# Kernel tuning notes

Measured on AMD Instinct MI355X. Metric: run time of the kernel, lower is better.

## Reference

```python
import jax, jax.numpy as jnp
import numpy as np
import math

DIM = 384
HEADS = 6
HID = 32  # PositionalEncodingFourier hidden_dim
B, H, W = 16, 56, 56


def _layer_norm(x, g, b, eps=1e-6):
    mu = jnp.mean(x, axis=-1, keepdims=True)
    var = jnp.mean((x - mu) ** 2, axis=-1, keepdims=True)
    return (x - mu) * jax.lax.rsqrt(var + eps) * g + b


def _pos_encoding_fourier(Bb, Hh, Ww, w, b):
    # EdgeNeXt PositionalEncodingFourier with all-False mask: cumsum == arange+1
    scale = 2.0 * math.pi
    y_embed = jnp.arange(1, Hh + 1, dtype=jnp.float32)[:, None] / (Hh + 1e-6) * scale
    x_embed = jnp.arange(1, Ww + 1, dtype=jnp.float32)[None, :] / (Ww + 1e-6) * scale
    dim_t = 10000.0 ** (2.0 * (jnp.arange(HID) // 2).astype(jnp.float32) / HID)
    def enc(e):
        p = jnp.broadcast_to(e, (Hh, Ww))[..., None] / dim_t  # (H,W,HID)
        return jnp.stack([jnp.sin(p[..., 0::2]), jnp.cos(p[..., 1::2])], axis=-1).reshape(Hh, Ww, HID)
    pos = jnp.concatenate([enc(y_embed), enc(x_embed)], axis=-1)  # (H,W,2*HID)
    pos = pos @ w.T + b  # 1x1 conv token_projection as matmul -> (H,W,DIM)
    return jnp.broadcast_to(jnp.transpose(pos, (2, 0, 1))[None], (Bb, DIM, Hh, Ww))


def _forward(x, pos_w, pos_b, ln_g, ln_b, gamma_xca, temperature,
             qkv_w, qkv_b, proj_w, proj_b, rpb_table, conv_w,
             bn_g, bn_b, bn_mean, bn_var, gamma):
    Bb, C, Hh, Ww = x.shape
    N = Hh * Ww
    d = C // HEADS
    xt = jnp.transpose(x.reshape(Bb, C, N), (0, 2, 1))  # (B,N,C)
    pos = _pos_encoding_fourier(Bb, Hh, Ww, pos_w, pos_b)
    xt = xt + jnp.transpose(pos.reshape(Bb, C, N), (0, 2, 1))

    # relative position bias (seq_len T=2): gather (T,T,h) -> expand (h,d^2,T,T)
    # -> nearest interp x0.5 selects element (0,0) -> pixel_shuffle(d) of constant
    # channels == per-head scalar broadcast over the (d,d) channel-attention map.
    T = 2
    rel_idx = jnp.arange(T)[:, None] - jnp.arange(T)[None, :] + T - 1  # (2,2)
    rpb = rpb_table[rel_idx.reshape(-1)].reshape(T, T, HEADS)
    bias = rpb[0, 0][None, :, None, None]  # (1,heads,1,1), broadcasts over (d,d)

    # XCA: cross-covariance (channel) attention
    xn = _layer_norm(xt, ln_g, ln_b)
    qkv = (xn @ qkv_w.T + qkv_b).reshape(Bb, N, 3, HEADS, d)
    qkv = jnp.transpose(qkv, (2, 0, 3, 4, 1))  # (3,B,h,d,N)
    q, k, v = qkv[0], qkv[1], qkv[2]
    q = q / jnp.maximum(jnp.linalg.norm(q, axis=-1, keepdims=True), 1e-12)
    k = k / jnp.maximum(jnp.linalg.norm(k, axis=-1, keepdims=True), 1e-12)
    attn = jnp.einsum('bhdn,bhen->bhde', q, k) * temperature + bias  # (B,h,d,d)
    attn = jax.nn.softmax(attn, axis=-1)
    out = jnp.einsum('bhde,bhen->bhdn', attn, v)  # (B,h,d,N)
    out = jnp.transpose(out, (0, 3, 1, 2)).reshape(Bb, N, C)
    out = out @ proj_w.T + proj_b
    xt = xt + gamma_xca * out

    x2 = jnp.transpose(xt, (0, 2, 1)).reshape(Bb, C, Hh, Ww)
    # pwconv0: conv3x3 (dim->dim, expan_ration hardcoded to 1) + BN(inference) + SiLU
    xi = jax.lax.conv_general_dilated(x2, conv_w, (1, 1), [(1, 1), (1, 1)],
                                      dimension_numbers=('NCHW', 'OIHW', 'NCHW'))
    xi = (xi - bn_mean[None, :, None, None]) * jax.lax.rsqrt(bn_var + 1e-5)[None, :, None, None]
    xi = xi * bn_g[None, :, None, None] + bn_b[None, :, None, None]
    xi = xi * jax.nn.sigmoid(xi)  # SiLU
    x2 = x2 + xi

    # faithful to source: raw reshape (NOT permute) of contiguous NCHW into (B,H,W,C)
    x3 = x2.reshape(Bb, Hh, Ww, C) * gamma
    x3 = jnp.transpose(x3, (0, 3, 1, 2))
    return x + x3


def setup_inputs() -> dict:
    key = jax.random.key(0)
    ks = jax.random.split(key, 10)
    d3 = 3 * DIM
    return {
        'x': jax.random.normal(ks[0], (B, DIM, H, W), jnp.float32),
        'pos_w': jax.random.normal(ks[1], (DIM, 2 * HID), jnp.float32) * 0.05,
        'pos_b': jnp.zeros((DIM,), jnp.float32),
        'ln_g': jnp.ones((DIM,), jnp.float32),
        'ln_b': jnp.zeros((DIM,), jnp.float32),
        'gamma_xca': jax.random.normal(ks[2], (DIM,), jnp.float32) * 0.1,
        'temperature': jnp.ones((HEADS, 1, 1), jnp.float32),
        'qkv_w': jax.random.normal(ks[3], (d3, DIM), jnp.float32) * (DIM ** -0.5),
        'qkv_b': jnp.zeros((d3,), jnp.float32),
        'proj_w': jax.random.normal(ks[4], (DIM, DIM), jnp.float32) * (DIM ** -0.5),
        'proj_b': jnp.zeros((DIM,), jnp.float32),
        'rpb_table': jax.random.normal(ks[5], (3, HEADS), jnp.float32) * 0.02,
        'conv_w': jax.random.normal(ks[6], (DIM, DIM, 3, 3), jnp.float32) * 0.02,
        'bn_g': jnp.ones((DIM,), jnp.float32),
        'bn_b': jnp.zeros((DIM,), jnp.float32),
        'bn_mean': jax.random.normal(ks[7], (DIM,), jnp.float32) * 0.1,
        'bn_var': jax.random.uniform(ks[8], (DIM,), jnp.float32, 0.5, 1.5),
        'gamma': jax.random.normal(ks[9], (DIM,), jnp.float32) * 0.1,
    }


def reference(x, pos_w, pos_b, ln_g, ln_b, gamma_xca, temperature,
              qkv_w, qkv_b, proj_w, proj_b, rpb_table, conv_w,
              bn_g, bn_b, bn_mean, bn_var, gamma):
    return _forward(x, pos_w, pos_b, ln_g, ln_b, gamma_xca, temperature,
                    qkv_w, qkv_b, proj_w, proj_b, rpb_table, conv_w,
                    bn_g, bn_b, bn_mean, bn_var, gamma)
```

## Files before the change

### kernel.cpp

```cpp
#include <hip/hip_runtime.h>
#include <hip/hip_bf16.h>
#include <math.h>

#define DIM 384
#define HEADS 6
#define NN 3136
#define BB 16
#define BH (BB*HEADS)
#define HP 58
#define NP (HP*HP)

typedef __attribute__((ext_vector_type(8))) short short8;
typedef __attribute__((ext_vector_type(4))) short short4v;
typedef __attribute__((ext_vector_type(4))) float f32x4;

__device__ __forceinline__ float bf2f(unsigned short u) {
    union { unsigned int i; float f; } v; v.i = ((unsigned int)u) << 16; return v.f;
}
__device__ __forceinline__ unsigned short f2bf(float f) {
    union { float f; unsigned int i; } v; v.f = f;
    unsigned int r = v.i + 0x7fffu + ((v.i >> 16) & 1u);
    return (unsigned short)(r >> 16);
}
__device__ __forceinline__ void glds16(const unsigned short* g, void* l) {
    __builtin_amdgcn_global_load_lds(
        (const __attribute__((address_space(1))) unsigned int*)g,
        (__attribute__((address_space(3))) unsigned int*)l, 16, 0, 0);
}

__global__ void kw_convert(const float* __restrict__ qkv_w, const float* __restrict__ proj_w,
                           const float* __restrict__ conv_w,
                           unsigned short* __restrict__ Wq, unsigned short* __restrict__ Wp,
                           unsigned short* __restrict__ Wc) {
    int tid = blockIdx.x * 256 + threadIdx.x;
    int stride = gridDim.x * 256;
    for (int i = tid; i < 3*DIM*DIM; i += stride) Wq[i] = f2bf(qkv_w[i]);
    for (int i = tid; i < DIM*DIM; i += stride) Wp[i] = f2bf(proj_w[i]);
    for (int i = tid; i < DIM*DIM*9; i += stride) {
        int ii = i % DIM; int rest = i / DIM; int tap = rest % 9; int o = rest / 9;
        Wc[i] = f2bf(conv_w[(size_t)(o*DIM + ii)*9 + tap]);
    }
}

__global__ void k_pos(const float* __restrict__ pos_w, const float* __restrict__ pos_b,
                      float* __restrict__ P) {
    int n = blockIdx.x; int h = n / 56, w = n % 56;
    __shared__ float feat[64];
    int t = threadIdx.x;
    if (t < 64) {
        int axis = t >> 5;
        int k = t & 31; int i = k >> 1;
        float e = (float)((axis ? w : h) + 1) / 56.000001f * 6.28318530717958647692f;
        float arg = e / powf(10000.0f, (float)i / 16.0f);
        feat[t] = (k & 1) ? cosf(arg) : sinf(arg);
    }
    __syncthreads();
    for (int c = t; c < DIM; c += blockDim.x) {
        float s = pos_b[c];
        #pragma unroll 8
        for (int k = 0; k < 64; k++) s += feat[k] * pos_w[c*64 + k];
        P[(size_t)n*DIM + c] = s;
    }
}

__global__ __launch_bounds__(256) void k_tln(const float* __restrict__ x, const float* __restrict__ P,
                                             const float* __restrict__ g, const float* __restrict__ be,
                                             unsigned short* __restrict__ XTb, unsigned short* __restrict__ XN) {
    __shared__ float tile[32][388];
    int blk = blockIdx.x;
    int b = blk / 98, nt = blk % 98;
    int n0 = nt*32;
    int t = threadIdx.x;
    #pragma unroll
    for (int it = 0; it < 12; it++) {
        int task = it*256 + t;
        int c = task >> 3, seg = task & 7;
        float4 v = *reinterpret_cast<const float4*>(x + ((size_t)(b*DIM + c))*NN + n0 + seg*4);
        tile[seg*4+0][c] = v.x; tile[seg*4+1][c] = v.y;
        tile[seg*4+2][c] = v.z; tile[seg*4+3][c] = v.w;
    }
    __syncthreads();
    int row = t >> 3, sub = t & 7;
    int n = n0 + row;
    f32x4 xp[12];
    float s = 0.f;
    #pragma unroll
    for (int k = 0; k < 12; k++) {
        int c0 = (k*8 + sub)*4;
        float4 tv = *reinterpret_cast<float4*>(&tile[row][c0]);
        float4 pv = *reinterpret_cast<const float4*>(P + (size_t)n*DIM + c0);
        f32x4 xv = {tv.x+pv.x, tv.y+pv.y, tv.z+pv.z, tv.w+pv.w};
        xp[k] = xv;
        s += xv[0]+xv[1]+xv[2]+xv[3];
        unsigned short pkx[4];
        #pragma unroll
        for (int e=0;e<4;e++) pkx[e] = f2bf(xv[e]);
        *reinterpret_cast<short4v*>(XTb + ((size_t)(b*NN + n))*DIM + c0) = *(short4v*)pkx;
    }
    s += __shfl_xor(s, 1, 64); s += __shfl_xor(s, 2, 64); s += __shfl_xor(s, 4, 64);
    float mean = s * (1.0f/384.0f);
    float sq = 0.f;
    #pragma unroll
    for (int k = 0; k < 12; k++) {
        #pragma unroll
        for (int e = 0; e < 4; e++) { float d = xp[k][e]-mean; sq += d*d; }
    }
    sq += __shfl_xor(sq, 1, 64); sq += __shfl_xor(sq, 2, 64); sq += __shfl_xor(sq, 4, 64);
    float rs = rsqrtf(sq * (1.0f/384.0f) + 1e-6f);
    #pragma unroll
    for (int k = 0; k < 12; k++) {
        int c0 = (k*8 + sub)*4;
        unsigned short pk[4];
        #pragma unroll
        for (int e = 0; e < 4; e++)
            pk[e] = f2bf((xp[k][e]-mean)*rs*g[c0+e] + be[c0+e]);
        *reinterpret_cast<short4v*>(XN + ((size_t)(b*NN + n))*DIM + c0) = *(short4v*)pk;
    }
}

template<int MODE>
__global__ __launch_bounds__(256) void k_gemm(
    const unsigned short* __restrict__ A, const unsigned short* __restrict__ Wt,
    const float* __restrict__ bias,
    unsigned short* __restrict__ Qb, unsigned short* __restrict__ Kb, unsigned short* __restrict__ Vt,
    const unsigned short* __restrict__ XTb, const float* __restrict__ gxca, unsigned short* __restrict__ X2p)
{
    __shared__ __align__(16) char smem[35328];
    auto ctA = (float(*)[69])smem;
    auto ctB = (float(*)[130])smem;

    constexpr int NCT = (MODE == 0) ? 9 : 3;
    constexpr int CPX = (MODE == 0) ? 441 : 147;
    int bid = blockIdx.x;
    int orig = (bid & 7)*CPX + (bid >> 3);
    int ct = orig % NCT, mt = orig / NCT;
    int m0 = mt*128, o0 = ct*128;
    int t = threadIdx.x;
    int wave = t >> 6, lane = t & 63;
    int wr = wave >> 1, wc = wave & 1;
    int lr = lane & 15, lg = lane >> 4;

    int r0 = t >> 2;
    int swcol = (((t & 3) ^ ((t >> 3) & 3)) << 3);
    const unsigned short* a0 = A  + (size_t)(m0 + r0)*384 + swcol;
    const unsigned short* a1 = A  + (size_t)(m0 + 64 + r0)*384 + swcol;
    const unsigned short* b0 = Wt + (size_t)(o0 + r0)*384 + swcol;
    const unsigned short* b1 = Wt + (size_t)(o0 + 64 + r0)*384 + swcol;
    int rsw = ((lr >> 1) & 3) << 3;

    auto stage = [&](char* base, int c) {
        glds16(a0 + c, base + wave*1024);
        glds16(a1 + c, base + 4096 + wave*1024);
        glds16(b0 + c, base + 8192 + wave*1024);
        glds16(b1 + c, base + 12288 + wave*1024);
    };

    f32x4 acc[4][4];
    #pragma unroll
    for (int i=0;i<4;i++) for (int j=0;j<4;j++) acc[i][j] = (f32x4){0.f,0.f,0.f,0.f};

    stage(smem, 0);
    __syncthreads();
    for (int kk = 0; kk < 12; kk++) {
        if (kk < 11) stage(smem + ((kk+1)&1)*16384, (kk+1)*32);
        auto As = (unsigned short(*)[32])(smem + (kk&1)*16384);
        auto Bs = (unsigned short(*)[32])(smem + (kk&1)*16384 + 8192);
        short8 af[4], bfv[4];
        #pragma unroll
        for (int i=0;i<4;i++) af[i]  = *(short8*)&As[wr*64 + i*16 + lr][(lg*8) ^ rsw];
        #pragma unroll
        for (int j=0;j<4;j++) bfv[j] = *(short8*)&Bs[wc*64 + j*16 + lr][(lg*8) ^ rsw];
        #pragma unroll
        for (int i=0;i<4;i++)
            #pragma unroll
            for (int j=0;j<4;j++)
                acc[i][j] = __builtin_amdgcn_mfma_f32_16x16x32_bf16(af[i], bfv[j], acc[i][j], 0, 0, 0);
        __syncthreads();
    }

    int comp = (MODE == 0) ? (o0 / DIM) : 0;
    for (int mh = 0; mh < 2; mh++) {
        __syncthreads();
        bool useB = (MODE == 1) || (MODE == 0 && comp == 2);
        if (wr == mh) {
            if (useB) {
                #pragma unroll
                for (int i=0;i<4;i++) for (int j=0;j<4;j++) for (int r=0;r<4;r++)
                    ctB[i*16 + lg*4 + r][wc*64 + j*16 + lr] = acc[i][j][r];
            } else {
                #pragma unroll
                for (int i=0;i<4;i++) for (int j=0;j<4;j++) for (int r=0;r<4;r++)
                    ctA[wc*64 + j*16 + lr][i*16 + lg*4 + r] = acc[i][j][r];
            }
        }
        __syncthreads();
        if (MODE == 1) {
            for (int q = t; q < 1024; q += 256) {
                int row = q >> 4, seg = q & 15;
                int m = m0 + mh*64 + row; int b = m/NN; int n = m - b*NN;
                int py = n/56, px = n - py*56;
                int og0 = o0 + seg*8;
                short8 xvb = *(const short8*)(XTb + (size_t)m*DIM + og0);
                unsigned short pk[8];
                #pragma unroll
                for (int e=0;e<8;e++) {
                    float val = ctB[row][seg*8+e] + bias[og0+e];
                    pk[e] = f2bf(bf2f((unsigned short)xvb[e]) + gxca[og0+e]*val);
                }
                *(short8*)(X2p + ((size_t)(b*NP + (py+1)*HP + px + 1))*DIM + og0) = *(short8*)pk;
            }
        } else if (comp < 2) {
            unsigned short* Dst = (comp == 0) ? Qb : Kb;
            for (int q = t; q < 2048; q += 256) {
                int row = q >> 4, seg = q & 15;
                int og = o0 + row; int rem = og - comp*DIM;
                int hh = rem >> 6, dd = rem & 63;
                int m4 = m0 + mh*64 + seg*4; int b = m4/NN; int n = m4 - b*NN;
                float bv = bias[og];
                unsigned short pk[4];
                #pragma unroll
                for (int e=0;e<4;e++) pk[e] = f2bf(ctA[row][seg*4+e] + bv);
                *(short4v*)(Dst + ((size_t)((b*HEADS + hh)*64 + dd))*NN + n) = *(short4v*)pk;
            }
        } else {
            for (int q = t; q < 1024; q += 256) {
                int row = q >> 4, seg = q & 15;
                int m = m0 + mh*64 + row; int b = m/NN; int n = m - b*NN;
                int og0 = o0 + seg*8; int rem0 = og0 - 2*DIM;
                int hh = rem0 >> 6, dd0 = rem0 & 63;
                unsigned short pk[8];
                #pragma unroll
                for (int e=0;e<8;e++) pk[e] = f2bf(ctB[row][seg*8+e] + bias[og0+e]);
                *(short8*)(Vt + ((size_t)((b*HEADS + hh)*NN + n))*64 + dd0) = *(short8*)pk;
            }
        }
    }
}

__global__ __launch_bounds__(256) void k_pad(unsigned short* __restrict__ X2p) {
    int b = blockIdx.x, part = blockIdx.y;
    unsigned short* base = X2p + (size_t)b*NP*DIM;
    short8 z = {0,0,0,0,0,0,0,0};
    for (int task = part*256 + threadIdx.x; task < 10944; task += 2048) {
        int pos = task / 48, seg = task - pos*48;
        int py, px;
        if (pos < 58)       { py = 0;  px = pos; }
        else if (pos < 116) { py = 57; px = pos - 58; }
        else if (pos < 172) { py = pos - 115; px = 0; }
        else                { py = pos - 171; px = 57; }
        *(short8*)(base + ((size_t)(py*HP + px))*DIM + seg*8) = z;
    }
}

__global__ __launch_bounds__(512) void k_conv(
    const unsigned short* __restrict__ A, const unsigned short* __restrict__ Wt,
    const float* __restrict__ bn_g, const float* __restrict__ bn_b,
    const float* __restrict__ bn_mean, const float* __restrict__ bn_var,
    float* __restrict__ Yout)
{
    __shared__ __align__(16) char smem[32768];
    auto ctA = (float(*)[69])smem;
    auto X2s = (unsigned short(*)[68])(smem + 17664);

    int bid = blockIdx.x;
    int orig = (bid & 7)*150 + (bid >> 3);
    int ct = orig % 3; int rest = orig / 3;
    int tile = rest % 25; int b = rest / 25;
    int n0 = tile*128, o0 = ct*128;
    int t = threadIdx.x;
    int wave = t >> 6, lane = t & 63;
    int wr = wave >> 2, wc = wave & 3;
    int lr = lane & 15, lg = lane >> 4;
    int qb = n0 + 2*(n0/56);
    const size_t bbase = (size_t)b*NP*DIM;

    int swcol = (((t & 3) ^ ((t >> 3) & 3)) << 3);
    const unsigned short* asrc[2];
    #pragma unroll
    for (int j=0;j<2;j++) {
        int row = j*128 + (t >> 2);
        int q = qb + row; if (q > NP-1) q = NP-1;
        asrc[j] = A + bbase + (size_t)q*DIM + swcol;
    }
    const unsigned short* bsrc = Wt + (size_t)(o0 + (t >> 2))*3456 + swcol;

    int qrel[4];
    #pragma unroll
    for (int i=0;i<4;i++) {
        int loc = wr*64 + i*16 + lr;
        int n = n0 + loc; if (n >= NN) n = NN-1;
        qrel[i] = n + 2*(n/56) - qb;
    }

    auto stageA = [&](int c) {
        #pragma unroll
        for (int j=0;j<2;j++) glds16(asrc[j] + c, smem + j*8192 + wave*1024);
    };
    auto stageB = [&](char* base, int off) {
        glds16(bsrc + off, base + wave*1024);
    };

    f32x4 acc[4][2];
    #pragma unroll
    for (int i=0;i<4;i++) for (int j=0;j<2;j++) acc[i][j] = (f32x4){0.f,0.f,0.f,0.f};

    stageA(0); stageB(smem + 16384, 0);
    __syncthreads();
    for (int kk = 0; kk < 12; kk++) {
        int c = kk*32;
        auto Ah = (unsigned short(*)[32])smem;
        #pragma unroll
        for (int tap = 0; tap < 9; tap++) {
            int buf = tap & 1;
            if (tap < 8) stageB(smem + 16384 + (buf^1)*8192, (tap+1)*384 + c);
            auto Bs = (unsigned short(*)[32])(smem + 16384 + buf*8192);
            int toff = (tap/3)*58 + (tap%3);
            short8 af[4], bfv[2];
            #pragma unroll
            for (int j=0;j<2;j++) {
                int brow = wc*32 + j*16 + lr;
                bfv[j] = *(short8*)&Bs[brow][(lg*8) ^ (((brow>>1)&3)<<3)];
            }
            #pragma unroll
            for (int i=0;i<4;i++) {
                int row = qrel[i] + toff;
                af[i] = *(short8*)&Ah[row][(lg*8) ^ (((row>>1)&3)<<3)];
            }
            #pragma unroll
            for (int i=0;i<4;i++)
                #pragma unroll
                for (int j=0;j<2;j++)
                    acc[i][j] = __builtin_amdgcn_mfma_f32_16x16x32_bf16(af[i], bfv[j], acc[i][j], 0, 0, 0);
            __syncthreads();
        }
        if (kk < 11) {
            stageA(c + 32);
            stageB(smem + 16384, c + 32);
            __syncthreads();
        }
    }

    for (int mh = 0; mh < 2; mh++) {
        for (int oh = 0; oh < 2; oh++) {
            __syncthreads();
            if (wr == mh && (wc >> 1) == oh) {
                #pragma unroll
                for (int i=0;i<4;i++) for (int j=0;j<2;j++) for (int r=0;r<4;r++)
                    ctA[(wc&1)*32 + j*16 + lr][i*16 + lg*4 + r] = acc[i][j][r];
            }
            {
                int row = t >> 3, sg = t & 7;
                int n = n0 + mh*64 + row; int nc = (n < NN) ? n : NN-1;
                int qq = nc + 2*(nc/56) + 59;
                short8 v = *(const short8*)(A + bbase + (size_t)qq*DIM + o0 + oh*64 + sg*8);
                short4v lo = {v[0],v[1],v[2],v[3]}, hi = {v[4],v[5],v[6],v[7]};
                *(short4v*)&X2s[row][sg*8]     = lo;
                *(short4v*)&X2s[row][sg*8 + 4] = hi;
            }
            __syncthreads();
            for (int q = t; q < 1024; q += 512) {
                int orow = q >> 4, sg = q & 15;
                int o = o0 + oh*64 + orow;
                int n = n0 + mh*64 + sg*4;
                if (n < NN) {
                    float mean = bn_mean[o], rs = rsqrtf(bn_var[o] + 1e-5f);
                    float gg = bn_g[o], bb2 = bn_b[o];
                    float4 ov; float* po = &ov.x;
                    #pragma unroll
                    for (int e=0;e<4;e++) {
                        float xi = (ctA[orow][sg*4+e] - mean)*rs*gg + bb2;
                        float si = xi / (1.0f + __expf(-xi));
                        po[e] = si + bf2f(X2s[sg*4+e][orow]);
                    }
                    *(float4*)(Yout + ((size_t)(b*DIM + o))*NN + n) = ov;
                }
            }
        }
    }
}

__global__ __launch_bounds__(256) void k_qk(const unsigned short* __restrict__ Qb,
                                            const unsigned short* __restrict__ Kb,
                                            float* __restrict__ Gp, float* __restrict__ Np) {
    int cx = blockIdx.x, bh = blockIdx.y;
    int t = threadIdx.x, wave = t >> 6, lane = t & 63;
    int lr = lane & 15, lg = lane >> 4;
    {
        int row = t >> 1, p = t & 1;
        const unsigned short* src = (row < 64)
            ? Qb + ((size_t)bh*64 + row)*NN + cx*448
            : Kb + ((size_t)bh*64 + (row-64))*NN + cx*448;
        float s = 0.f;
        #pragma unroll
        for (int it = 0; it < 28; it++) {
            short8 v = *(const short8*)(src + p*224 + it*8);
            #pragma unroll
            for (int jj=0;jj<8;jj++) { float f = bf2f((unsigned short)v[jj]); s += f*f; }
        }
        s += __shfl_xor(s, 1, 64);
        if (p == 0) Np[((size_t)bh*7 + cx)*128 + row] = s;
    }
    f32x4 acc[4];
    #pragma unroll
    for (int j=0;j<4;j++) acc[j] = (f32x4){0.f,0.f,0.f,0.f};
    const unsigned short* qrow = Qb + ((size_t)bh*64 + wave*16 + lr)*NN + cx*448;
    const unsigned short* kbase = Kb + (size_t)bh*64*NN + cx*448;
    for (int ks = 0; ks < 14; ks++) {
        short8 a = *(const short8*)(qrow + ks*32 + lg*8);
        #pragma unroll
        for (int j=0;j<4;j++) {
            short8 bfr = *(const short8*)(kbase + (size_t)(j*16+lr)*NN + ks*32 + lg*8);
            acc[j] = __builtin_amdgcn_mfma_f32_16x16x32_bf16(a, bfr, acc[j], 0, 0, 0);
        }
    }
    float* gbase = Gp + ((size_t)bh*7 + cx)*4096;
    #pragma unroll
    for (int j=0;j<4;j++)
        #pragma unroll
        for (int r=0;r<4;r++)
            gbase[(wave*16 + lg*4 + r)*64 + j*16 + lr] = acc[j][r];
}

__global__ __launch_bounds__(256) void k_sm(const float* __restrict__ Gp, const float* __restrict__ Np,
                                            const float* __restrict__ temperature,
                                            const float* __restrict__ rpb,
                                            unsigned short* __restrict__ ATT) {
    int bh = blockIdx.x; int h = bh % HEADS;
    int t = threadIdx.x;
    __shared__ float snorm[128];
    if (t < 128) {
        float s = 0.f;
        #pragma unroll
        for (int cx=0;cx<7;cx++) s += Np[((size_t)bh*7 + cx)*128 + t];
        snorm[t] = fmaxf(sqrtf(s), 1e-12f);
    }
    __syncthreads();
    int dq = t >> 2, de0 = (t & 3) * 16;
    f32x4 g[4];
    #pragma unroll
    for (int i=0;i<4;i++) g[i] = (f32x4){0.f,0.f,0.f,0.f};
    #pragma unroll
    for (int cx=0;cx<7;cx++) {
        const float* base = Gp + ((size_t)bh*7 + cx)*4096 + dq*64 + de0;
        #pragma unroll
        for (int i=0;i<4;i++) {
            float4 v = *(const float4*)(base + i*4);
            g[i][0]+=v.x; g[i][1]+=v.y; g[i][2]+=v.z; g[i][3]+=v.w;
        }
    }
    float temp = temperature[h];
    float bias = rpb[HEADS + h];
    float qn = snorm[dq];
    float lv[16]; float mx = -1e30f;
    #pragma unroll
    for (int i=0;i<4;i++)
        #pragma unroll
        for (int e=0;e<4;e++) {
            int de = de0 + i*4 + e;
            float v = g[i][e] / (qn * snorm[64 + de]) * temp + bias;
            lv[i*4+e] = v; mx = fmaxf(mx, v);
        }
    mx = fmaxf(mx, __shfl_xor(mx, 1, 64));
    mx = fmaxf(mx, __shfl_xor(mx, 2, 64));
    float se = 0.f;
    #pragma unroll
    for (int e=0;e<16;e++) { lv[e] = __expf(lv[e]-mx); se += lv[e]; }
    se += __shfl_xor(se, 1, 64);
    se += __shfl_xor(se, 2, 64);
    float inv = 1.0f/se;
    unsigned short pk[16];
    #pragma unroll
    for (int e=0;e<16;e++) pk[e] = f2bf(lv[e]*inv);
    unsigned short* dst = ATT + ((size_t)bh*64 + dq)*64 + de0;
    *(short8*)dst       = *(short8*)pk;
    *(short8*)(dst + 8) = *(short8*)(pk + 8);
}

__global__ __launch_bounds__(256) void k_pv(const unsigned short* __restrict__ ATT,
                                            const unsigned short* __restrict__ Vt,
                                            unsigned short* __restrict__ XCA) {
    int nt = blockIdx.x, bh = blockIdx.y;
    int b = bh / HEADS, h = bh % HEADS;
    int t = threadIdx.x, wave = t >> 6, lane = t & 63;
    int lr = lane & 15, lg = lane >> 4;
    int n0 = nt*64;
    __shared__ float ctP[64][67];
    f32x4 acc[4];
    for (int i=0;i<4;i++) acc[i] = (f32x4){0.f,0.f,0.f,0.f};
    for (int ks=0; ks<2; ks++) {
        short8 bfr = *reinterpret_cast<const short8*>(Vt + ((size_t)bh*NN + n0 + wave*16 + lr)*64 + ks*32 + lg*8);
        for (int i=0;i<4;i++) {
            short8 a = *reinterpret_cast<const short8*>(ATT + ((size_t)bh*64 + i*16 + lr)*64 + ks*32 + lg*8);
            acc[i] = __builtin_amdgcn_mfma_f32_16x16x32_bf16(a, bfr, acc[i], 0, 0, 0);
        }
    }
    int nl = wave*16 + lr;
    #pragma unroll
    for (int i=0;i<4;i++)
        #pragma unroll
        for (int r=0;r<4;r++) ctP[nl][i*16 + lg*4 + r] = acc[i][r];
    __syncthreads();
    for (int q = t; q < 512; q += 256) {
        int row = q >> 3, seg = q & 7;
        unsigned short pk[8];
        #pragma unroll
        for (int e=0;e<8;e++) pk[e] = f2bf(ctP[row][seg*8+e]);
        *(short8*)(XCA + ((size_t)(b*NN + n0 + row))*DIM + h*64 + seg*8) = *(short8*)pk;
    }
}

__global__ __launch_bounds__(256) void k_final(const float* __restrict__ x, const float* __restrict__ Y,
                                               const float* __restrict__ gamma, float* __restrict__ out) {
    int i = blockIdx.x, b = blockIdx.y, kc = blockIdx.z;
    __shared__ float tile[56*193];
    int t = threadIdx.x;
    int k0 = kc*192;
    const float* ybase = Y + (size_t)b*DIM*NN + (size_t)i*21504 + k0;
    for (int q = t; q < 56*48; q += 256) {
        int j = q / 48, c4 = (q % 48) * 4;
        float4 v = *reinterpret_cast<const float4*>(ybase + (size_t)j*384 + c4);
        float* dst = &tile[j*193 + c4];
        dst[0]=v.x; dst[1]=v.y; dst[2]=v.z; dst[3]=v.w;
    }
    __syncthreads();
    for (int q = t; q < 192*56; q += 256) {
        int kl = q / 56, j = q % 56;
        int k = k0 + kl;
        size_t gi = ((size_t)(b*DIM + k))*NN + (size_t)i*56 + j;
        out[gi] = x[gi] + gamma[k] * tile[j*193 + kl];
    }
}

extern "C" void kernel_launch(void* const* d_in, const int* in_sizes, int n_in,
                              void* d_out, int out_size, void* d_ws, size_t ws_size,
                              hipStream_t stream) {
    const float* x       = (const float*)d_in[0];
    const float* pos_w   = (const float*)d_in[1];
    const float* pos_b   = (const float*)d_in[2];
    const float* ln_g    = (const float*)d_in[3];
    const float* ln_b    = (const float*)d_in[4];
    const float* gxca    = (const float*)d_in[5];
    const float* temp    = (const float*)d_in[6];
    const float* qkv_w   = (const float*)d_in[7];
    const float* qkv_b   = (const float*)d_in[8];
    const float* proj_w  = (const float*)d_in[9];
    const float* proj_b  = (const float*)d_in[10];
    const float* rpb     = (const float*)d_in[11];
    const float* conv_w  = (const float*)d_in[12];
    const float* bn_g    = (const float*)d_in[13];
    const float* bn_b    = (const float*)d_in[14];
    const float* bn_mean = (const float*)d_in[15];
    const float* bn_var  = (const float*)d_in[16];
    const float* gamma   = (const float*)d_in[17];
    float* out = (float*)d_out;
    char* ws = (char*)d_ws;

    const size_t oP   = 0;
    const size_t oXT  = oP   + 4816896;
    const size_t oXN  = oXT  + 77070336;
    const size_t oQ   = oXN  + 38535168;
    const size_t oK   = oQ   + 38535168;
    const size_t oV   = oK   + 38535168;
    const size_t oATT = oV   + 38535168;
    const size_t oWq  = oATT + 786432;
    const size_t oWp  = oWq  + 884736;
    const size_t oWc  = oWp  + 294912;

    float* P            = (float*)(ws + oP);
    unsigned short* XTb = (unsigned short*)(ws + oXT);
    float* Y            = (float*)(ws + oXT);
    unsigned short* XN  = (unsigned short*)(ws + oXN);
    float* Gp           = (float*)(ws + oXN);
    float* Np           = (float*)(ws + oXN + 11010048);
    unsigned short* XCA = (unsigned short*)(ws + oXN);
    unsigned short* Qb  = (unsigned short*)(ws + oQ);
    unsigned short* X2p = (unsigned short*)(ws + oQ);
    unsigned short* Kb  = (unsigned short*)(ws + oK);
    unsigned short* Vt  = (unsigned short*)(ws + oV);
    unsigned short* ATT = (unsigned short*)(ws + oATT);
    unsigned short* Wq  = (unsigned short*)(ws + oWq);
    unsigned short* Wp  = (unsigned short*)(ws + oWp);
    unsigned short* Wc  = (unsigned short*)(ws + oWc);

    kw_convert<<<256, 256, 0, stream>>>(qkv_w, proj_w, conv_w, Wq, Wp, Wc);
    k_pos<<<NN, 128, 0, stream>>>(pos_w, pos_b, P);
    k_tln<<<BB*98, 256, 0, stream>>>(x, P, ln_g, ln_b, XTb, XN);
    k_gemm<0><<<3528, 256, 0, stream>>>(XN, Wq, qkv_b,
        Qb, Kb, Vt, nullptr, nullptr, nullptr);
    k_qk<<<dim3(7, BH), 256, 0, stream>>>(Qb, Kb, Gp, Np);
    k_sm<<<BH, 256, 0, stream>>>(Gp, Np, temp, rpb, ATT);
    k_pad<<<dim3(BB, 8), 256, 0, stream>>>(X2p);
    k_pv<<<dim3(49, BH), 256, 0, stream>>>(ATT, Vt, XCA);
    k_gemm<1><<<1176, 256, 0, stream>>>(XCA, Wp, proj_b,
        nullptr, nullptr, nullptr, XTb, gxca, X2p);
    k_conv<<<1200, 512, 0, stream>>>(X2p, Wc, bn_g, bn_b, bn_mean, bn_var, Y);
    k_final<<<dim3(56, BB, 2), 256, 0, stream>>>(x, Y, gamma, out);
}
```

Before: 505.8 us.

## Use 4-wave conv blocks with larger per-wave tiles and bf16 intermediate output

```diff
diff --git a/kernel.cpp b/kernel.cpp
--- a/kernel.cpp
+++ b/kernel.cpp
@@ -252,11 +252,11 @@
     }
 }
 
-__global__ __launch_bounds__(512) void k_conv(
+__global__ __launch_bounds__(256, 3) void k_conv(
     const unsigned short* __restrict__ A, const unsigned short* __restrict__ Wt,
     const float* __restrict__ bn_g, const float* __restrict__ bn_b,
     const float* __restrict__ bn_mean, const float* __restrict__ bn_var,
-    float* __restrict__ Yout)
+    unsigned short* __restrict__ Yout)
 {
     __shared__ __align__(16) char smem[32768];
     auto ctA = (float(*)[69])smem;
@@ -269,20 +269,22 @@
     int n0 = tile*128, o0 = ct*128;
     int t = threadIdx.x;
     int wave = t >> 6, lane = t & 63;
-    int wr = wave >> 2, wc = wave & 3;
+    int wr = wave >> 1, wc = wave & 1;
     int lr = lane & 15, lg = lane >> 4;
     int qb = n0 + 2*(n0/56);
     const size_t bbase = (size_t)b*NP*DIM;
 
     int swcol = (((t & 3) ^ ((t >> 3) & 3)) << 3);
-    const unsigned short* asrc[2];
-    #pragma unroll
-    for (int j=0;j<2;j++) {
-        int row = j*128 + (t >> 2);
+    const unsigned short* asrc[4];
+    #pragma unroll
+    for (int j=0;j<4;j++) {
+        int task = j*256 + t;
+        int row = task >> 2;
         int q = qb + row; if (q > NP-1) q = NP-1;
         asrc[j] = A + bbase + (size_t)q*DIM + swcol;
     }
-    const unsigned short* bsrc = Wt + (size_t)(o0 + (t >> 2))*3456 + swcol;
+    const unsigned short* bsrc0 = Wt + (size_t)(o0 + (t>>2))*3456 + swcol;
+    const unsigned short* bsrc1 = Wt + (size_t)(o0 + 64 + (t>>2))*3456 + swcol;
 
     int qrel[4];
     #pragma unroll
@@ -294,15 +296,16 @@
 
     auto stageA = [&](int c) {
         #pragma unroll
-        for (int j=0;j<2;j++) glds16(asrc[j] + c, smem + j*8192 + wave*1024);
+        for (int j=0;j<4;j++) glds16(asrc[j] + c, smem + j*4096 + wave*1024);
     };
     auto stageB = [&](char* base, int off) {
-        glds16(bsrc + off, base + wave*1024);
+        glds16(bsrc0 + off, base + wave*1024);
+        glds16(bsrc1 + off, base + 4096 + wave*1024);
     };
 
-    f32x4 acc[4][2];
-    #pragma unroll
-    for (int i=0;i<4;i++) for (int j=0;j<2;j++) acc[i][j] = (f32x4){0.f,0.f,0.f,0.f};
+    f32x4 acc[4][4];
+    #pragma unroll
+    for (int i=0;i<4;i++) for (int j=0;j<4;j++) acc[i][j] = (f32x4){0.f,0.f,0.f,0.f};
 
     stageA(0); stageB(smem + 16384, 0);
     __syncthreads();
@@ -315,10 +318,10 @@
             if (tap < 8) stageB(smem + 16384 + (buf^1)*8192, (tap+1)*384 + c);
             auto Bs = (unsigned short(*)[32])(smem + 16384 + buf*8192);
             int toff = (tap/3)*58 + (tap%3);
-            short8 af[4], bfv[2];
+            short8 af[4], bfv[4];
             #pragma unroll
-            for (int j=0;j<2;j++) {
-                int brow = wc*32 + j*16 + lr;
+            for (int j=0;j<4;j++) {
+                int brow = wc*64 + j*16 + lr;
                 bfv[j] = *(short8*)&Bs[brow][(lg*8) ^ (((brow>>1)&3)<<3)];
             }
             #pragma unroll
@@ -329,7 +332,7 @@
             #pragma unroll
             for (int i=0;i<4;i++)
                 #pragma unroll
-                for (int j=0;j<2;j++)
+                for (int j=0;j<4;j++)
                     acc[i][j] = __builtin_amdgcn_mfma_f32_16x16x32_bf16(af[i], bfv[j], acc[i][j], 0, 0, 0);
             __syncthreads();
         }
@@ -343,13 +346,13 @@
     for (int mh = 0; mh < 2; mh++) {
         for (int oh = 0; oh < 2; oh++) {
             __syncthreads();
-            if (wr == mh && (wc >> 1) == oh) {
+            if (wr == mh && wc == oh) {
                 #pragma unroll
-                for (int i=0;i<4;i++) for (int j=0;j<2;j++) for (int r=0;r<4;r++)
-                    ctA[(wc&1)*32 + j*16 + lr][i*16 + lg*4 + r] = acc[i][j][r];
-            }
-            {
-                int row = t >> 3, sg = t & 7;
+                for (int i=0;i<4;i++) for (int j=0;j<4;j++) for (int r=0;r<4;r++)
+                    ctA[j*16 + lr][i*16 + lg*4 + r] = acc[i][j][r];
+            }
+            for (int q = t; q < 512; q += 256) {
+                int row = q >> 3, sg = q & 7;
                 int n = n0 + mh*64 + row; int nc = (n < NN) ? n : NN-1;
                 int qq = nc + 2*(nc/56) + 59;
                 short8 v = *(const short8*)(A + bbase + (size_t)qq*DIM + o0 + oh*64 + sg*8);
@@ -358,21 +361,21 @@
                 *(short4v*)&X2s[row][sg*8 + 4] = hi;
             }
             __syncthreads();
-            for (int q = t; q < 1024; q += 512) {
-                int orow = q >> 4, sg = q & 15;
+            for (int q = t; q < 512; q += 256) {
+                int orow = q >> 3, sg = q & 7;
                 int o = o0 + oh*64 + orow;
-                int n = n0 + mh*64 + sg*4;
+                int n = n0 + mh*64 + sg*8;
                 if (n < NN) {
                     float mean = bn_mean[o], rs = rsqrtf(bn_var[o] + 1e-5f);
                     float gg = bn_g[o], bb2 = bn_b[o];
-                    float4 ov; float* po = &ov.x;
+                    unsigned short pk[8];
                     #pragma unroll
-                    for (int e=0;e<4;e++) {
-                        float xi = (ctA[orow][sg*4+e] - mean)*rs*gg + bb2;
+                    for (int e=0;e<8;e++) {
+                        float xi = (ctA[orow][sg*8+e] - mean)*rs*gg + bb2;
                         float si = xi / (1.0f + __expf(-xi));
-                        po[e] = si + bf2f(X2s[sg*4+e][orow]);
+                        pk[e] = f2bf(si + bf2f(X2s[sg*8+e][orow]));
                     }
-                    *(float4*)(Yout + ((size_t)(b*DIM + o))*NN + n) = ov;
+                    *(short8*)(Yout + ((size_t)(b*DIM + o))*NN + n) = *(short8*)pk;
                 }
             }
         }
@@ -509,18 +512,19 @@
     }
 }
 
-__global__ __launch_bounds__(256) void k_final(const float* __restrict__ x, const float* __restrict__ Y,
+__global__ __launch_bounds__(256) void k_final(const float* __restrict__ x, const unsigned short* __restrict__ Yb,
                                                const float* __restrict__ gamma, float* __restrict__ out) {
     int i = blockIdx.x, b = blockIdx.y, kc = blockIdx.z;
     __shared__ float tile[56*193];
     int t = threadIdx.x;
     int k0 = kc*192;
-    const float* ybase = Y + (size_t)b*DIM*NN + (size_t)i*21504 + k0;
-    for (int q = t; q < 56*48; q += 256) {
-        int j = q / 48, c4 = (q % 48) * 4;
-        float4 v = *reinterpret_cast<const float4*>(ybase + (size_t)j*384 + c4);
-        float* dst = &tile[j*193 + c4];
-        dst[0]=v.x; dst[1]=v.y; dst[2]=v.z; dst[3]=v.w;
+    const unsigned short* ybase = Yb + (size_t)b*DIM*NN + (size_t)i*21504 + k0;
+    for (int q = t; q < 56*24; q += 256) {
+        int j = q / 24, c8 = (q % 24) * 8;
+        short8 v = *(const short8*)(ybase + (size_t)j*384 + c8);
+        float* dst = &tile[j*193 + c8];
+        #pragma unroll
+        for (int e=0;e<8;e++) dst[e] = bf2f((unsigned short)v[e]);
     }
     __syncthreads();
     for (int q = t; q < 192*56; q += 256) {
@@ -568,7 +572,7 @@
 
     float* P            = (float*)(ws + oP);
     unsigned short* XTb = (unsigned short*)(ws + oXT);
-    float* Y            = (float*)(ws + oXT);
+    unsigned short* Yb  = (unsigned short*)(ws + oXT);
     unsigned short* XN  = (unsigned short*)(ws + oXN);
     float* Gp           = (float*)(ws + oXN);
     float* Np           = (float*)(ws + oXN + 11010048);
@@ -593,6 +597,6 @@
     k_pv<<<dim3(49, BH), 256, 0, stream>>>(ATT, Vt, XCA);
     k_gemm<1><<<1176, 256, 0, stream>>>(XCA, Wp, proj_b,
         nullptr, nullptr, nullptr, XTb, gxca, X2p);
-    k_conv<<<1200, 512, 0, stream>>>(X2p, Wc, bn_g, bn_b, bn_mean, bn_var, Y);
-    k_final<<<dim3(56, BB, 2), 256, 0, stream>>>(x, Y, gamma, out);
-}
+    k_conv<<<1200, 256, 0, stream>>>(X2p, Wc, bn_g, bn_b, bn_mean, bn_var, Yb);
+    k_final<<<dim3(56, BB, 2), 256, 0, stream>>>(x, Yb, gamma, out);
+}
```

Result: faster. 474.1 us (-6.3%).
